# Kernel optimization log

Measured on AMD Instinct MI355X. Metric: run time of the kernel, lower is better.

## Reference

```python
import jax, jax.numpy as jnp
import numpy as np

NUM_NODES = 50000
NUM_EDGES = 600000
NUM_FEAT = 128
HIDDEN = 512
N_OUT = 128
K = 3
N_GRAPHS = 128


def setup_inputs() -> dict:
    key = jax.random.key(0)
    ks = jax.random.split(key, 12)
    feature = jax.random.normal(ks[0], (NUM_NODES, NUM_FEAT), dtype=jnp.float32)
    edge_index = jax.random.randint(ks[1], (2, NUM_EDGES), 0, NUM_NODES, dtype=jnp.int64)
    protein_batch = jnp.sort(jax.random.randint(ks[2], (NUM_NODES,), 0, N_GRAPHS, dtype=jnp.int64))
    s = 0.05
    # ChebConv weights stored [K, in, out] (x @ W), single shared bias per conv
    W1 = jax.random.normal(ks[3], (K, NUM_FEAT, NUM_FEAT), dtype=jnp.float32) * s
    b1 = jax.random.normal(ks[4], (NUM_FEAT,), dtype=jnp.float32) * s
    W2 = jax.random.normal(ks[5], (K, NUM_FEAT, 2 * NUM_FEAT), dtype=jnp.float32) * s
    b2 = jax.random.normal(ks[6], (2 * NUM_FEAT,), dtype=jnp.float32) * s
    fc1_w = jax.random.normal(ks[7], (3 * NUM_FEAT, HIDDEN), dtype=jnp.float32) * s
    fc1_b = jax.random.normal(ks[8], (HIDDEN,), dtype=jnp.float32) * s
    fc2_w = jax.random.normal(ks[9], (HIDDEN, N_OUT), dtype=jnp.float32) * s
    fc2_b = jax.random.normal(ks[10], (N_OUT,), dtype=jnp.float32) * s
    return {"feature": feature, "edge_index": edge_index, "protein_batch": protein_batch,
            "W1": W1, "b1": b1, "W2": W2, "b2": b2,
            "fc1_w": fc1_w, "fc1_b": fc1_b, "fc2_w": fc2_w, "fc2_b": fc2_b}


def _cheb_conv(x, src, dst, edge_w, W, b):
    # PyG ChebConv with sym normalization, lambda_max=2 => scaled Laplacian
    # L_hat has zero diagonal and off-diag weights -1/sqrt(d_i d_j) (edge_w).
    def prop(h):
        return jax.ops.segment_sum(edge_w[:, None] * h[src], dst, num_segments=NUM_NODES)

    Tx0 = x
    out = Tx0 @ W[0]
    Tx1 = prop(x)
    out = out + Tx1 @ W[1]
    for k in range(2, W.shape[0]):
        Tx2 = 2.0 * prop(Tx1) - Tx0
        out = out + Tx2 @ W[k]
        Tx0, Tx1 = Tx1, Tx2
    return out + b


def reference(feature, edge_index, protein_batch, W1, b1, W2, b2, fc1_w, fc1_b, fc2_w, fc2_b):
    src, dst = edge_index[0], edge_index[1]
    deg = jax.ops.segment_sum(jnp.ones_like(src, dtype=feature.dtype), src, num_segments=NUM_NODES)
    dinv = jnp.where(deg > 0, jax.lax.rsqrt(jnp.maximum(deg, 1.0)), 0.0)
    edge_w = -dinv[src] * dinv[dst]  # (2/lambda_max)*L_sym off-diagonal; diag cancels to 0

    gx = jax.nn.relu(_cheb_conv(feature, src, dst, edge_w, W1, b1))
    gx = jax.nn.relu(_cheb_conv(gx, src, dst, edge_w, W2, b2))
    gx = jnp.concatenate([gx, feature], axis=1)  # [N, 3*F]

    # global_mean_pool
    sums = jax.ops.segment_sum(gx, protein_batch, num_segments=N_GRAPHS)
    cnts = jax.ops.segment_sum(jnp.ones((gx.shape[0],), gx.dtype), protein_batch, num_segments=N_GRAPHS)
    pooled = sums / jnp.maximum(cnts, 1.0)[:, None]

    h = jax.nn.relu(pooled @ fc1_w + fc1_b)  # dropout is identity in eval
    return h @ fc2_w + fc2_b
```

## Files before the change

kernel.cpp:

```cpp
#include <hip/hip_runtime.h>
#include <hip/hip_bf16.h>

#define NNODES 50000
#define NEDGES 600000
#define NB 196
#define NBKT 196
#define SB 192
#define SCH (NEDGES / SB)

typedef short vs8 __attribute__((ext_vector_type(8)));
typedef float floatx4 __attribute__((ext_vector_type(4)));

__device__ __forceinline__ float us2f(unsigned short u) {
    unsigned int x = ((unsigned int)u) << 16;
    float f;
    __builtin_memcpy(&f, &x, 4);
    return f;
}
__device__ __forceinline__ unsigned short f2us(float f) {
    unsigned int x;
    __builtin_memcpy(&x, &f, 4);
    unsigned int r = x + 0x7fffu + ((x >> 16) & 1u);
    return (unsigned short)(r >> 16);
}
__device__ __forceinline__ float ldf(const void* p, int i, int ff) {
    if (ff) return us2f(((const unsigned short*)p)[i]);
    return ((const float*)p)[i];
}
__device__ __forceinline__ int2 ldnt_sw(const int2* p) {
    unsigned long long v =
        __builtin_nontemporal_load(reinterpret_cast<const unsigned long long*>(p));
    int2 r;
    r.x = (int)(unsigned int)(v & 0xffffffffULL);
    r.y = (int)(unsigned int)(v >> 32);
    return r;
}
__device__ __forceinline__ void gload_lds16(const unsigned short* g, unsigned short* l) {
    __builtin_amdgcn_global_load_lds(
        (const __attribute__((address_space(1))) unsigned int*)g,
        (__attribute__((address_space(3))) unsigned int*)l, 16, 0, 0);
}
__device__ __forceinline__ void accum8(float w, uint4 u, float& a0, float& a1,
                                       float& a2, float& a3, float& a4, float& a5,
                                       float& a6, float& a7) {
    a0 += w * us2f((unsigned short)(u.x & 0xffffu));
    a1 += w * us2f((unsigned short)(u.x >> 16));
    a2 += w * us2f((unsigned short)(u.y & 0xffffu));
    a3 += w * us2f((unsigned short)(u.y >> 16));
    a4 += w * us2f((unsigned short)(u.z & 0xffffu));
    a5 += w * us2f((unsigned short)(u.z >> 16));
    a6 += w * us2f((unsigned short)(u.w & 0xffffu));
    a7 += w * us2f((unsigned short)(u.w >> 16));
}

__global__ void k_detect(const int* ei, const unsigned int* fw, int* iflag, int* fflag) {
    int lane = threadIdx.x;
    int odd1 = ei[2 * lane + 1];
    int odd2 = ei[128 + 2 * lane + 1];
    unsigned long long nz = __ballot(odd1 != 0 || odd2 != 0);
    unsigned int e = (fw[lane] >> 7) & 0xffu;
    unsigned long long h = __ballot(e > 100u && e < 160u);
    if (lane == 0) {
        *iflag = (nz == 0ULL) ? 1 : 0;
        *fflag = (__popcll(h) > 40) ? 1 : 0;
    }
}

__global__ void k_init(const int* pb, const int* iflag, int* b32, float* psum) {
    int i = blockIdx.x * 256 + threadIdx.x;
    if (i < NNODES) {
        int f = *iflag;
        b32[i] = pb[((size_t)i) << f];
    }
    if (i < 128 * 384) psum[i] = 0.f;
}

__global__ __launch_bounds__(256) void k_deghist(const int* ei, const int* iflag,
                                                 unsigned int* degpart, int* cntpart) {
    __shared__ unsigned int h[25000];
    __shared__ int c[NBKT];
    int t = threadIdx.x, blk = blockIdx.x;
    for (int i = t; i < 25000; i += 256) h[i] = 0u;
    if (t < NBKT) c[t] = 0;
    __syncthreads();
    int f = *iflag;
    int e0 = blk * SCH;
    for (int j = t; j < SCH; j += 256) {
        int e = e0 + j;
        int s = ei[((size_t)e) << f];
        int d = ei[((size_t)(NEDGES + e)) << f];
        atomicAdd(&h[s >> 1], (s & 1) ? 65536u : 1u);
        atomicAdd(&c[d >> 8], 1);
    }
    __syncthreads();
    unsigned int* dp = degpart + (size_t)blk * 25000;
    for (int i = t; i < 25000; i += 256) dp[i] = h[i];
    if (t < NBKT) cntpart[blk * NBKT + t] = c[t];
}

__global__ void k_dred(const unsigned int* degpart, float* dinv) {
    int i = blockIdx.x * 256 + threadIdx.x;
    if (i >= 25000) return;
    unsigned int lo = 0, hi = 0;
    for (int b = 0; b < SB; ++b) {
        unsigned int p = degpart[(size_t)b * 25000 + i];
        lo += p & 0xffffu;
        hi += p >> 16;
    }
    dinv[2 * i] = lo ? rsqrtf((float)lo) : 0.f;
    dinv[2 * i + 1] = hi ? rsqrtf((float)hi) : 0.f;
}

__global__ void k_bscan(const int* cntpart, int* bbase, int* gbase,
                        const int* batch32, int* pcnt, int* rowptr) {
    __shared__ int tot[256];
    int t = threadIdx.x;
    int sum = 0;
    if (t < NBKT) {
        for (int b = 0; b < SB; ++b) sum += cntpart[b * NBKT + t];
    }
    tot[t] = sum;
    __syncthreads();
    for (int off = 1; off < 256; off <<= 1) {
        int x = (t >= off) ? tot[t - off] : 0;
        __syncthreads();
        tot[t] += x;
        __syncthreads();
    }
    int excl = tot[t] - sum;
    if (t < NBKT) {
        gbase[t] = excl;
        int run = excl;
        for (int b = 0; b < SB; ++b) {
            bbase[b * NBKT + t] = run;
            run += cntpart[b * NBKT + t];
        }
    }
    if (t == 0) {
        gbase[NBKT] = NEDGES;
        rowptr[NNODES] = NEDGES;
    }
    if (t < 128) {
        int g = t;
        int lo = 0, hi = NNODES;
        while (lo < hi) { int mid = (lo + hi) >> 1; if (batch32[mid] < g) lo = mid + 1; else hi = mid; }
        int start = lo;
        hi = NNODES;
        while (lo < hi) { int mid = (lo + hi) >> 1; if (batch32[mid] <= g) lo = mid + 1; else hi = mid; }
        pcnt[g] = lo - start;
    }
}

__global__ void k_scat(const int* ei, const int* iflag, const float* dinv,
                       const int* bbase, int2* bkt) {
    __shared__ int cur[NBKT];
    int t = threadIdx.x, blk = blockIdx.x;
    if (t < NBKT) cur[t] = bbase[blk * NBKT + t];
    __syncthreads();
    int f = *iflag;
    int e0 = blk * SCH;
    for (int j = t; j < SCH; j += 256) {
        int e = e0 + j;
        int s = ei[((size_t)e) << f];
        int d = ei[((size_t)(NEDGES + e)) << f];
        float w = -dinv[s] * dinv[d];
        int slot = atomicAdd(&cur[d >> 8], 1);
        int wb;
        __builtin_memcpy(&wb, &w, 4);
        int2 v;
        v.x = s | ((d & 255) << 16);
        v.y = wb;
        bkt[slot] = v;
    }
}

__global__ void k_csr(const int2* bkt, const int* gbase, int* rowptr, int2* csr_sw) {
    __shared__ int hist[256], scan[256], cur[256];
    int t = threadIdx.x, b = blockIdx.x;
    int beg = gbase[b], end = gbase[b + 1];
    int n = end - beg;
    hist[t] = 0;
    __syncthreads();
    for (int i = t; i < n; i += 256) {
        int bin = (bkt[beg + i].x >> 16) & 255;
        atomicAdd(&hist[bin], 1);
    }
    __syncthreads();
    int h = hist[t];
    scan[t] = h;
    __syncthreads();
    for (int off = 1; off < 256; off <<= 1) {
        int x = (t >= off) ? scan[t - off] : 0;
        __syncthreads();
        scan[t] += x;
        __syncthreads();
    }
    int excl = scan[t] - h;
    int node = b * 256 + t;
    if (node < NNODES) rowptr[node] = beg + excl;
    cur[t] = excl;
    __syncthreads();
    for (int i = t; i < n; i += 256) {
        int2 p = bkt[beg + i];
        int bin = (p.x >> 16) & 255;
        int slot = atomicAdd(&cur[bin], 1);
        int2 v;
        v.x = p.x & 0xffff;
        v.y = p.y;
        csr_sw[beg + slot] = v;
    }
}

__global__ void k_featb(const void* src, const int* fflag, unsigned short* dst) {
    int i = blockIdx.x * 256 + threadIdx.x;
    if (i >= NNODES * 128 / 8) return;
    if (*fflag) {
        reinterpret_cast<uint4*>(dst)[i] = reinterpret_cast<const uint4*>(src)[i];
    } else {
        const float4* fs = reinterpret_cast<const float4*>(src);
        float4 a = fs[2 * i], b = fs[2 * i + 1];
        uint4 o;
        o.x = (unsigned int)f2us(a.x) | ((unsigned int)f2us(a.y) << 16);
        o.y = (unsigned int)f2us(a.z) | ((unsigned int)f2us(a.w) << 16);
        o.z = (unsigned int)f2us(b.x) | ((unsigned int)f2us(b.y) << 16);
        o.w = (unsigned int)f2us(b.z) | ((unsigned int)f2us(b.w) << 16);
        reinterpret_cast<uint4*>(dst)[i] = o;
    }
}

__global__ void k_trans2(const void* W1, const void* W2, const int* fflag,
                         unsigned short* W1t, unsigned short* W2t) {
    int idx = blockIdx.x * 256 + threadIdx.x;
    int ff = *fflag;
    if (idx < 49152) {
        int c = idx >> 13;
        int rem = idx & 8191;
        int cr = rem >> 6;
        int rem2 = rem & 63;
        int g = rem2 >> 3, j = rem2 & 7;
        int k = c * 64 + ((g ^ (cr & 7)) << 3) + j;
        int n = cr;
        float v;
        if (k < 128) v = ldf(W1, k * 128 + n, ff) - ldf(W1, (256 + k) * 128 + n, ff);
        else if (k < 256) v = ldf(W1, k * 128 + n, ff);
        else v = 2.f * ldf(W1, k * 128 + n, ff);
        W1t[idx] = f2us(v);
    } else if (idx < 49152 + 98304) {
        int jx = idx - 49152;
        int ct = jx / 49152;
        int rem = jx % 49152;
        int c = rem >> 13;
        int rem1 = rem & 8191;
        int cr = rem1 >> 6;
        int rem2 = rem1 & 63;
        int g = rem2 >> 3, j = rem2 & 7;
        int k = c * 64 + ((g ^ (cr & 7)) << 3) + j;
        int n = ct * 128 + cr;
        float v;
        if (k < 128) v = ldf(W2, k * 256 + n, ff) - ldf(W2, (256 + k) * 256 + n, ff);
        else if (k < 256) v = ldf(W2, k * 256 + n, ff);
        else v = 2.f * ldf(W2, k * 256 + n, ff);
        W2t[jx] = f2us(v);
    }
}

__global__ void k_prepw(const void* b1, const void* b2, const void* f1w, const void* f1b,
                        const void* f2w, const void* f2b, const int* fflag,
                        float* b1f, float* b2f, float* f1wf, float* f1bf,
                        float* f2wf, float* f2bf) {
    int i = blockIdx.x * 256 + threadIdx.x;
    int ff = *fflag;
    if (i < 196608) { f1wf[i] = ldf(f1w, i, ff); return; }
    i -= 196608;
    if (i < 65536) { f2wf[i] = ldf(f2w, i, ff); return; }
    i -= 65536;
    if (i < 512) { f1bf[i] = ldf(f1b, i, ff); return; }
    i -= 512;
    if (i < 256) { b2f[i] = ldf(b2, i, ff); return; }
    i -= 256;
    if (i < 128) { b1f[i] = ldf(b1, i, ff); return; }
    i -= 128;
    if (i < 128) f2bf[i] = ldf(f2b, i, ff);
}

__global__ __launch_bounds__(256, 8) void k_prop(const unsigned short* X,
                                                 const int* rowptr, const int2* csr_sw,
                                                 unsigned short* out) {
    int wvid = (blockIdx.x * blockDim.x + threadIdx.x) >> 6;
    int lane = threadIdx.x & 63;
    int q = lane >> 4;
    int ln = lane & 15;
    int node = wvid * 4 + q;
    if (node >= NNODES) return;
    int fo = ln * 8;
    int beg = rowptr[node], end = rowptr[node + 1];
    float a0 = 0.f, a1 = 0.f, a2 = 0.f, a3 = 0.f;
    float a4 = 0.f, a5 = 0.f, a6 = 0.f, a7 = 0.f;
    int j = beg;
    for (; j + 4 <= end; j += 4) {
        int2 e0 = ldnt_sw(csr_sw + j);
        int2 e1 = ldnt_sw(csr_sw + j + 1);
        int2 e2 = ldnt_sw(csr_sw + j + 2);
        int2 e3 = ldnt_sw(csr_sw + j + 3);
        uint4 u0 = *reinterpret_cast<const uint4*>(X + (size_t)e0.x * 128 + fo);
        uint4 u1 = *reinterpret_cast<const uint4*>(X + (size_t)e1.x * 128 + fo);
        uint4 u2 = *reinterpret_cast<const uint4*>(X + (size_t)e2.x * 128 + fo);
        uint4 u3 = *reinterpret_cast<const uint4*>(X + (size_t)e3.x * 128 + fo);
        float w0, w1, w2, w3;
        __builtin_memcpy(&w0, &e0.y, 4);
        __builtin_memcpy(&w1, &e1.y, 4);
        __builtin_memcpy(&w2, &e2.y, 4);
        __builtin_memcpy(&w3, &e3.y, 4);
        accum8(w0, u0, a0, a1, a2, a3, a4, a5, a6, a7);
        accum8(w1, u1, a0, a1, a2, a3, a4, a5, a6, a7);
        accum8(w2, u2, a0, a1, a2, a3, a4, a5, a6, a7);
        accum8(w3, u3, a0, a1, a2, a3, a4, a5, a6, a7);
    }
    for (; j < end; ++j) {
        int2 e = ldnt_sw(csr_sw + j);
        float w;
        __builtin_memcpy(&w, &e.y, 4);
        uint4 u = *reinterpret_cast<const uint4*>(X + (size_t)e.x * 128 + fo);
        accum8(w, u, a0, a1, a2, a3, a4, a5, a6, a7);
    }
    uint4 ov;
    ov.x = (unsigned int)f2us(a0) | ((unsigned int)f2us(a1) << 16);
    ov.y = (unsigned int)f2us(a2) | ((unsigned int)f2us(a3) << 16);
    ov.z = (unsigned int)f2us(a4) | ((unsigned int)f2us(a5) << 16);
    ov.w = (unsigned int)f2us(a6) | ((unsigned int)f2us(a7) << 16);
    *reinterpret_cast<uint4*>(out + (size_t)node * 128 + fo) = ov;
}

template <int POOL, int CT>
__global__ __launch_bounds__(512, 4) void k_convg(
    const unsigned short* seg0, const unsigned short* seg1, const unsigned short* seg2,
    const unsigned short* Wt, const float* bias, unsigned short* out,
    const int* batch32, float* psum) {
    __shared__ __align__(16) unsigned short a_lds[2][8192];
    __shared__ __align__(16) unsigned short b_lds[2][8192];
    __shared__ float sh_ps[POOL ? 1024 : 1];
    int tid = threadIdx.x;
    int bid = blockIdx.x;
    int grp = 8 * CT;
    int main_blocks = 48 * grp;
    int r, ct;
    if (bid < main_blocks) {
        int g = bid / grp;
        int rem = bid - g * grp;
        ct = rem >> 3;
        r = g * 8 + (rem & 7);
    } else {
        int t = bid - main_blocks;
        r = 384 + (CT == 1 ? t : t % 7);
        ct = (CT == 1) ? 0 : t / 7;
    }
    int r0 = r * 128;
    const unsigned short* segs[3] = {seg0, seg1, seg2};
    int wv = tid >> 6, lane = tid & 63;
    int wm = wv >> 2, wn = wv & 3;
    int m = lane & 15, kq = lane >> 4;
    if (POOL) { sh_ps[tid] = 0.f; sh_ps[tid + 512] = 0.f; }

    auto STAGE = [&](int buf, int c) {
        const unsigned short* S = segs[c >> 1];
        int h = c & 1;
#pragma unroll
        for (int p = 0; p < 2; ++p) {
            int q = wv * 2 + p;
            int rl = q * 8 + (lane >> 3);
            int g = lane & 7;
            int rowg = r0 + rl;
            if (rowg >= NNODES) rowg = NNODES - 1;
            gload_lds16(S + (size_t)rowg * 128 + h * 64 + ((g ^ (rl & 7)) << 3),
                        &a_lds[buf][q * 512]);
        }
#pragma unroll
        for (int p = 0; p < 2; ++p) {
            int q = wv * 2 + p;
            gload_lds16(Wt + (size_t)(ct * 6 + c) * 8192 + q * 512 + (lane << 3),
                        &b_lds[buf][q * 512]);
        }
    };

    floatx4 acc[4][2];
#pragma unroll
    for (int mt = 0; mt < 4; ++mt)
#pragma unroll
        for (int nt = 0; nt < 2; ++nt) {
            acc[mt][nt][0] = 0.f; acc[mt][nt][1] = 0.f;
            acc[mt][nt][2] = 0.f; acc[mt][nt][3] = 0.f;
        }

    STAGE(0, 0);
    __syncthreads();
    int buf = 0;
#pragma unroll
    for (int c = 0; c < 6; ++c) {
        if (c < 5) STAGE(buf ^ 1, c + 1);
        vs8 af[4], bfr[2];
#pragma unroll
        for (int kf = 0; kf < 2; ++kf) {
            int G = kf * 4 + kq;
#pragma unroll
            for (int mt = 0; mt < 4; ++mt) {
                int row = wm * 64 + mt * 16 + m;
                af[mt] = *reinterpret_cast<const vs8*>(
                    &a_lds[buf][row * 64 + ((G ^ (row & 7)) << 3)]);
            }
#pragma unroll
            for (int nt = 0; nt < 2; ++nt) {
                int cl = wn * 32 + nt * 16 + m;
                bfr[nt] = *reinterpret_cast<const vs8*>(
                    &b_lds[buf][cl * 64 + ((G ^ (cl & 7)) << 3)]);
            }
#pragma unroll
            for (int mt = 0; mt < 4; ++mt)
#pragma unroll
                for (int nt = 0; nt < 2; ++nt)
                    acc[mt][nt] = __builtin_amdgcn_mfma_f32_16x16x32_bf16(
                        af[mt], bfr[nt], acc[mt][nt], 0, 0, 0);
        }
        if (c < 5) {
            __syncthreads();
            buf ^= 1;
        }
    }

    if (POOL == 0) {
#pragma unroll
        for (int mt = 0; mt < 4; ++mt) {
            int rbase = r0 + wm * 64 + mt * 16 + kq * 4;
#pragma unroll
            for (int nt = 0; nt < 2; ++nt) {
                int col = wn * 32 + nt * 16 + m;
                float bv = bias[col];
#pragma unroll
                for (int i = 0; i < 4; ++i) {
                    int rw = rbase + i;
                    if (rw < NNODES) {
                        float v = acc[mt][nt][i] + bv;
                        v = v > 0.f ? v : 0.f;
                        out[(size_t)rw * 128 + col] = f2us(v);
                    }
                }
            }
        }
    } else {
        int g0 = batch32[r0];
#pragma unroll
        for (int mt = 0; mt < 4; ++mt) {
            int rbase = r0 + wm * 64 + mt * 16 + kq * 4;
            int gid[4];
#pragma unroll
            for (int i = 0; i < 4; ++i) {
                int rw = rbase + i;
                gid[i] = rw < NNODES ? batch32[rw] : -1;
            }
#pragma unroll
            for (int nt = 0; nt < 2; ++nt) {
                int cl = wn * 32 + nt * 16 + m;
                int col = ct * 128 + cl;
                float bv = bias[col];
                float run = 0.f;
                int curg = -1;
#pragma unroll
                for (int i = 0; i < 4; ++i) {
                    int g = gid[i];
                    if (g < 0) break;
                    float v = acc[mt][nt][i] + bv;
                    v = v > 0.f ? v : 0.f;
                    if (g != curg) {
                        if (curg >= 0) {
                            int gl = curg - g0;
                            if (gl >= 0 && gl < 8) atomicAdd(&sh_ps[gl * 128 + cl], run);
                            else atomicAdd(&psum[curg * 384 + col], run);
                        }
                        curg = g;
                        run = 0.f;
                    }
                    run += v;
                }
                if (curg >= 0) {
                    int gl = curg - g0;
                    if (gl >= 0 && gl < 8) atomicAdd(&sh_ps[gl * 128 + cl], run);
                    else atomicAdd(&psum[curg * 384 + col], run);
                }
            }
        }
        __syncthreads();
        for (int idx = tid; idx < 1024; idx += 512) {
            int gl = idx >> 7, cl = idx & 127;
            float v = sh_ps[idx];
            int gg = g0 + gl;
            if (v != 0.f && gg < 128) atomicAdd(&psum[(size_t)gg * 384 + ct * 128 + cl], v);
        }
    }
}

__global__ void k_poolnodes(const unsigned short* featb, const int* batch32, float* psum) {
    int col = threadIdx.x & 127;
    int half = threadIdx.x >> 7;
    int nbeg = blockIdx.x * 128 + half * 64;
    if (nbeg >= NNODES) return;
    int nend = nbeg + 64;
    if (nend > NNODES) nend = NNODES;
    float run = 0.f;
    int curg = batch32[nbeg];
    for (int n = nbeg; n < nend; ++n) {
        int g = batch32[n];
        if (g != curg) {
            atomicAdd(&psum[curg * 384 + 256 + col], run);
            run = 0.f;
            curg = g;
        }
        run += us2f(featb[(size_t)n * 128 + col]);
    }
    atomicAdd(&psum[curg * 384 + 256 + col], run);
}

__global__ void k_fc1(const float* psum, const int* pcnt, const float* w,
                      const float* b, float* h) {
    int g = blockIdx.x, j = threadIdx.x * 2;
    int c = pcnt[g];
    float inv = 1.f / (float)(c > 0 ? c : 1);
    float a0 = 0.f, a1 = 0.f;
    for (int k = 0; k < 384; ++k) {
        float p = psum[g * 384 + k];
        a0 += p * w[k * 512 + j];
        a1 += p * w[k * 512 + j + 1];
    }
    a0 = a0 * inv + b[j];
    a1 = a1 * inv + b[j + 1];
    h[g * 512 + j] = a0 > 0.f ? a0 : 0.f;
    h[g * 512 + j + 1] = a1 > 0.f ? a1 : 0.f;
}

__global__ void ChebModel_74380243632480_kernel(const float* h, const float* w,
                                                const float* b, const int* fflag,
                                                void* out) {
    int g = blockIdx.x, j = threadIdx.x;
    float acc = 0.f;
    for (int k = 0; k < 512; ++k) acc += h[g * 512 + k] * w[k * 128 + j];
    acc += b[j];
    if (*fflag) ((unsigned short*)out)[g * 128 + j] = f2us(acc);
    else ((float*)out)[g * 128 + j] = acc;
}

extern "C" void kernel_launch(void* const* d_in, const int* in_sizes, int n_in,
                              void* d_out, int out_size, void* d_ws, size_t ws_size,
                              hipStream_t stream) {
    const void* feature = d_in[0];
    const int* edge_index = (const int*)d_in[1];
    const int* batch = (const int*)d_in[2];
    const void* W1 = d_in[3];
    const void* b1 = d_in[4];
    const void* W2 = d_in[5];
    const void* b2 = d_in[6];
    const void* fc1w = d_in[7];
    const void* fc1b = d_in[8];
    const void* fc2w = d_in[9];
    const void* fc2b = d_in[10];

    char* ws = (char*)d_ws;
    size_t off = 0;
    int* iflag = (int*)(ws + off); off += 256;
    int* fflag = (int*)(ws + off); off += 256;
    int* rowptr = (int*)(ws + off); off += ((size_t)(NNODES + 1) * 4 + 255) & ~(size_t)255;
    float* dinv = (float*)(ws + off); off += ((size_t)NNODES * 4 + 255) & ~(size_t)255;
    int* batch32 = (int*)(ws + off); off += ((size_t)NNODES * 4 + 255) & ~(size_t)255;
    int* gbase = (int*)(ws + off); off += 1024;
    int* cntpart = (int*)(ws + off); off += ((size_t)SB * NBKT * 4 + 255) & ~(size_t)255;
    int* bbase = (int*)(ws + off); off += ((size_t)SB * NBKT * 4 + 255) & ~(size_t)255;
    int2* csr_sw = (int2*)(ws + off); off += ((size_t)NEDGES * 8 + 255) & ~(size_t)255;
    unsigned short* featb = (unsigned short*)(ws + off); off += ((size_t)NNODES * 128 * 2 + 255) & ~(size_t)255;
    unsigned short* T1 = (unsigned short*)(ws + off); off += ((size_t)NNODES * 128 * 2 + 255) & ~(size_t)255;
    unsigned short* T2 = (unsigned short*)(ws + off); off += ((size_t)NNODES * 128 * 2 + 255) & ~(size_t)255;
    unsigned short* gx1 = (unsigned short*)(ws + off); off += ((size_t)NNODES * 128 * 2 + 255) & ~(size_t)255;
    unsigned short* W1t = (unsigned short*)(ws + off); off += ((size_t)49152 * 2 + 255) & ~(size_t)255;
    unsigned short* W2t = (unsigned short*)(ws + off); off += ((size_t)98304 * 2 + 255) & ~(size_t)255;
    float* b1f = (float*)(ws + off); off += 1024;
    float* b2f = (float*)(ws + off); off += 1024;
    float* fc1wf = (float*)(ws + off); off += ((size_t)196608 * 4 + 255) & ~(size_t)255;
    float* fc1bf = (float*)(ws + off); off += 2048;
    float* fc2wf = (float*)(ws + off); off += ((size_t)65536 * 4 + 255) & ~(size_t)255;
    float* fc2bf = (float*)(ws + off); off += 1024;
    float* psum = (float*)(ws + off); off += ((size_t)128 * 384 * 4 + 255) & ~(size_t)255;
    int* pcnt = (int*)(ws + off); off += 1024;
    float* hbuf = (float*)(ws + off); off += ((size_t)128 * 512 * 4 + 255) & ~(size_t)255;

    int2* bkt = (int2*)T1;
    unsigned int* degpart = (unsigned int*)T2;

    k_detect<<<1, 64, 0, stream>>>(edge_index, (const unsigned int*)feature, iflag, fflag);
    k_init<<<(NNODES + 255) / 256, 256, 0, stream>>>(batch, iflag, batch32, psum);
    k_deghist<<<SB, 256, 0, stream>>>(edge_index, iflag, degpart, cntpart);
    k_dred<<<(25000 + 255) / 256, 256, 0, stream>>>(degpart, dinv);
    k_bscan<<<1, 256, 0, stream>>>(cntpart, bbase, gbase, batch32, pcnt, rowptr);
    k_scat<<<SB, 256, 0, stream>>>(edge_index, iflag, dinv, bbase, bkt);
    k_csr<<<NBKT, 256, 0, stream>>>(bkt, gbase, rowptr, csr_sw);

    k_featb<<<(NNODES * 128 / 8 + 255) / 256, 256, 0, stream>>>(feature, fflag, featb);
    k_trans2<<<(49152 + 98304 + 255) / 256, 256, 0, stream>>>(W1, W2, fflag, W1t, W2t);
    k_prepw<<<(263168 + 255) / 256, 256, 0, stream>>>(b1, b2, fc1w, fc1b, fc2w, fc2b, fflag,
                                                      b1f, b2f, fc1wf, fc1bf, fc2wf, fc2bf);

    int pb = ((NNODES + 3) / 4 * 64 + 255) / 256;
    k_prop<<<pb, 256, 0, stream>>>(featb, rowptr, csr_sw, T1);
    k_prop<<<pb, 256, 0, stream>>>(T1, rowptr, csr_sw, T2);
    k_convg<0, 1><<<391, 512, 0, stream>>>(featb, T1, T2, W1t, b1f, gx1,
                                           (const int*)0, (float*)0);
    k_prop<<<pb, 256, 0, stream>>>(gx1, rowptr, csr_sw, T1);
    k_prop<<<pb, 256, 0, stream>>>(T1, rowptr, csr_sw, T2);
    k_convg<1, 2><<<782, 512, 0, stream>>>(gx1, T1, T2, W2t, b2f, (unsigned short*)0,
                                           batch32, psum);
    k_poolnodes<<<(NNODES + 127) / 128, 256, 0, stream>>>(featb, batch32, psum);
    k_fc1<<<128, 256, 0, stream>>>(psum, pcnt, fc1wf, fc1bf, hbuf);
    ChebModel_74380243632480_kernel<<<128, 128, 0, stream>>>(hbuf, fc2wf, fc2bf, fflag, d_out);
}
```

Measured before the change: 393.1 us.

## Fuse setup kernels, parallelize bucket prefix scan, unroll SpMM gather by eight

Merges the batch/psum init into the feature bf16 conversion kernel and the three weight-prep kernels into one, cutting kernel launches. Replaces the single-block serial per-bucket scan over 192 partitions with a transposed count layout, a parallel per-bucket prefix kernel and a small global scan, so k_scat computes its base offsets directly. The propagation kernel gains an 8-way unrolled edge loop with more gathers in flight, and its launch-bounds occupancy hint drops from 8 to 6 to leave room for the extra registers. The risks are higher register pressure and lower occupancy in the hot gather kernel.

Result: faster. 367.2 us (-6.6%).

```diff
diff --git a/kernel.cpp b/kernel.cpp
--- a/kernel.cpp
+++ b/kernel.cpp
@@ -66,17 +66,31 @@
     }
 }
 
-__global__ void k_init(const int* pb, const int* iflag, int* b32, float* psum) {
+__global__ void k_featb(const void* src, const int* iflag, const int* fflag,
+                        const int* pb, int* b32, float* psum, unsigned short* dst) {
     int i = blockIdx.x * 256 + threadIdx.x;
     if (i < NNODES) {
         int f = *iflag;
         b32[i] = pb[((size_t)i) << f];
     }
     if (i < 128 * 384) psum[i] = 0.f;
+    if (i >= NNODES * 128 / 8) return;
+    if (*fflag) {
+        reinterpret_cast<uint4*>(dst)[i] = reinterpret_cast<const uint4*>(src)[i];
+    } else {
+        const float4* fs = reinterpret_cast<const float4*>(src);
+        float4 a = fs[2 * i], b = fs[2 * i + 1];
+        uint4 o;
+        o.x = (unsigned int)f2us(a.x) | ((unsigned int)f2us(a.y) << 16);
+        o.y = (unsigned int)f2us(a.z) | ((unsigned int)f2us(a.w) << 16);
+        o.z = (unsigned int)f2us(b.x) | ((unsigned int)f2us(b.y) << 16);
+        o.w = (unsigned int)f2us(b.z) | ((unsigned int)f2us(b.w) << 16);
+        reinterpret_cast<uint4*>(dst)[i] = o;
+    }
 }
 
 __global__ __launch_bounds__(256) void k_deghist(const int* ei, const int* iflag,
-                                                 unsigned int* degpart, int* cntpart) {
+                                                 unsigned int* degpart, int* cntT) {
     __shared__ unsigned int h[25000];
     __shared__ int c[NBKT];
     int t = threadIdx.x, blk = blockIdx.x;
@@ -95,7 +109,7 @@
     __syncthreads();
     unsigned int* dp = degpart + (size_t)blk * 25000;
     for (int i = t; i < 25000; i += 256) dp[i] = h[i];
-    if (t < NBKT) cntpart[blk * NBKT + t] = c[t];
+    if (t < NBKT) cntT[t * SB + blk] = c[t];
 }
 
 __global__ void k_dred(const unsigned int* degpart, float* dinv) {
@@ -111,31 +125,36 @@
     dinv[2 * i + 1] = hi ? rsqrtf((float)hi) : 0.f;
 }
 
-__global__ void k_bscan(const int* cntpart, int* bbase, int* gbase,
-                        const int* batch32, int* pcnt, int* rowptr) {
-    __shared__ int tot[256];
+__global__ void k_bprefix(int* cntT, int* btot) {
+    __shared__ int sh[256];
+    int t = threadIdx.x, b = blockIdx.x;
+    int v = (t < SB) ? cntT[b * SB + t] : 0;
+    sh[t] = v;
+    __syncthreads();
+    for (int off = 1; off < 256; off <<= 1) {
+        int x = (t >= off) ? sh[t - off] : 0;
+        __syncthreads();
+        sh[t] += x;
+        __syncthreads();
+    }
+    if (t < SB) cntT[b * SB + t] = sh[t] - v;
+    if (t == 255) btot[b] = sh[255];
+}
+
+__global__ void k_bscan2(const int* btot, int* gbase, const int* batch32,
+                         int* pcnt, int* rowptr) {
+    __shared__ int sh[256];
     int t = threadIdx.x;
-    int sum = 0;
-    if (t < NBKT) {
-        for (int b = 0; b < SB; ++b) sum += cntpart[b * NBKT + t];
-    }
-    tot[t] = sum;
+    int v = (t < NBKT) ? btot[t] : 0;
+    sh[t] = v;
     __syncthreads();
     for (int off = 1; off < 256; off <<= 1) {
-        int x = (t >= off) ? tot[t - off] : 0;
+        int x = (t >= off) ? sh[t - off] : 0;
         __syncthreads();
-        tot[t] += x;
+        sh[t] += x;
         __syncthreads();
     }
-    int excl = tot[t] - sum;
-    if (t < NBKT) {
-        gbase[t] = excl;
-        int run = excl;
-        for (int b = 0; b < SB; ++b) {
-            bbase[b * NBKT + t] = run;
-            run += cntpart[b * NBKT + t];
-        }
-    }
+    if (t < NBKT) gbase[t] = sh[t] - v;
     if (t == 0) {
         gbase[NBKT] = NEDGES;
         rowptr[NNODES] = NEDGES;
@@ -152,10 +171,10 @@
 }
 
 __global__ void k_scat(const int* ei, const int* iflag, const float* dinv,
-                       const int* bbase, int2* bkt) {
+                       const int* gbase, const int* cntT, int2* bkt) {
     __shared__ int cur[NBKT];
     int t = threadIdx.x, blk = blockIdx.x;
-    if (t < NBKT) cur[t] = bbase[blk * NBKT + t];
+    if (t < NBKT) cur[t] = gbase[t] + cntT[t * SB + blk];
     __syncthreads();
     int f = *iflag;
     int e0 = blk * SCH;
@@ -211,30 +230,16 @@
     }
 }
 
-__global__ void k_featb(const void* src, const int* fflag, unsigned short* dst) {
+__global__ void k_prepall(const void* W1, const void* W2, const void* b1, const void* b2,
+                          const void* f1w, const void* f1b, const void* f2w, const void* f2b,
+                          const int* fflag, unsigned short* W1t, unsigned short* W2t,
+                          float* b1f, float* b2f, float* f1wf, float* f1bf,
+                          float* f2wf, float* f2bf) {
     int i = blockIdx.x * 256 + threadIdx.x;
-    if (i >= NNODES * 128 / 8) return;
-    if (*fflag) {
-        reinterpret_cast<uint4*>(dst)[i] = reinterpret_cast<const uint4*>(src)[i];
-    } else {
-        const float4* fs = reinterpret_cast<const float4*>(src);
-        float4 a = fs[2 * i], b = fs[2 * i + 1];
-        uint4 o;
-        o.x = (unsigned int)f2us(a.x) | ((unsigned int)f2us(a.y) << 16);
-        o.y = (unsigned int)f2us(a.z) | ((unsigned int)f2us(a.w) << 16);
-        o.z = (unsigned int)f2us(b.x) | ((unsigned int)f2us(b.y) << 16);
-        o.w = (unsigned int)f2us(b.z) | ((unsigned int)f2us(b.w) << 16);
-        reinterpret_cast<uint4*>(dst)[i] = o;
-    }
-}
-
-__global__ void k_trans2(const void* W1, const void* W2, const int* fflag,
-                         unsigned short* W1t, unsigned short* W2t) {
-    int idx = blockIdx.x * 256 + threadIdx.x;
     int ff = *fflag;
-    if (idx < 49152) {
-        int c = idx >> 13;
-        int rem = idx & 8191;
+    if (i < 49152) {
+        int c = i >> 13;
+        int rem = i & 8191;
         int cr = rem >> 6;
         int rem2 = rem & 63;
         int g = rem2 >> 3, j = rem2 & 7;
@@ -244,11 +249,13 @@
         if (k < 128) v = ldf(W1, k * 128 + n, ff) - ldf(W1, (256 + k) * 128 + n, ff);
         else if (k < 256) v = ldf(W1, k * 128 + n, ff);
         else v = 2.f * ldf(W1, k * 128 + n, ff);
-        W1t[idx] = f2us(v);
-    } else if (idx < 49152 + 98304) {
-        int jx = idx - 49152;
-        int ct = jx / 49152;
-        int rem = jx % 49152;
+        W1t[i] = f2us(v);
+        return;
+    }
+    i -= 49152;
+    if (i < 98304) {
+        int ct = i / 49152;
+        int rem = i % 49152;
         int c = rem >> 13;
         int rem1 = rem & 8191;
         int cr = rem1 >> 6;
@@ -260,16 +267,10 @@
         if (k < 128) v = ldf(W2, k * 256 + n, ff) - ldf(W2, (256 + k) * 256 + n, ff);
         else if (k < 256) v = ldf(W2, k * 256 + n, ff);
         else v = 2.f * ldf(W2, k * 256 + n, ff);
-        W2t[jx] = f2us(v);
-    }
-}
-
-__global__ void k_prepw(const void* b1, const void* b2, const void* f1w, const void* f1b,
-                        const void* f2w, const void* f2b, const int* fflag,
-                        float* b1f, float* b2f, float* f1wf, float* f1bf,
-                        float* f2wf, float* f2bf) {
-    int i = blockIdx.x * 256 + threadIdx.x;
-    int ff = *fflag;
+        W2t[i] = f2us(v);
+        return;
+    }
+    i -= 98304;
     if (i < 196608) { f1wf[i] = ldf(f1w, i, ff); return; }
     i -= 196608;
     if (i < 65536) { f2wf[i] = ldf(f2w, i, ff); return; }
@@ -283,7 +284,7 @@
     if (i < 128) f2bf[i] = ldf(f2b, i, ff);
 }
 
-__global__ __launch_bounds__(256, 8) void k_prop(const unsigned short* X,
+__global__ __launch_bounds__(256, 6) void k_prop(const unsigned short* X,
                                                  const int* rowptr, const int2* csr_sw,
                                                  unsigned short* out) {
     int wvid = (blockIdx.x * blockDim.x + threadIdx.x) >> 6;
@@ -297,6 +298,41 @@
     float a0 = 0.f, a1 = 0.f, a2 = 0.f, a3 = 0.f;
     float a4 = 0.f, a5 = 0.f, a6 = 0.f, a7 = 0.f;
     int j = beg;
+    for (; j + 8 <= end; j += 8) {
+        int2 e0 = ldnt_sw(csr_sw + j);
+        int2 e1 = ldnt_sw(csr_sw + j + 1);
+        int2 e2 = ldnt_sw(csr_sw + j + 2);
+        int2 e3 = ldnt_sw(csr_sw + j + 3);
+        int2 e4 = ldnt_sw(csr_sw + j + 4);
+        int2 e5 = ldnt_sw(csr_sw + j + 5);
+        int2 e6 = ldnt_sw(csr_sw + j + 6);
+        int2 e7 = ldnt_sw(csr_sw + j + 7);
+        uint4 u0 = *reinterpret_cast<const uint4*>(X + (size_t)e0.x * 128 + fo);
+        uint4 u1 = *reinterpret_cast<const uint4*>(X + (size_t)e1.x * 128 + fo);
+        uint4 u2 = *reinterpret_cast<const uint4*>(X + (size_t)e2.x * 128 + fo);
+        uint4 u3 = *reinterpret_cast<const uint4*>(X + (size_t)e3.x * 128 + fo);
+        uint4 u4 = *reinterpret_cast<const uint4*>(X + (size_t)e4.x * 128 + fo);
+        uint4 u5 = *reinterpret_cast<const uint4*>(X + (size_t)e5.x * 128 + fo);
+        uint4 u6 = *reinterpret_cast<const uint4*>(X + (size_t)e6.x * 128 + fo);
+        uint4 u7 = *reinterpret_cast<const uint4*>(X + (size_t)e7.x * 128 + fo);
+        float w0, w1, w2, w3, w4, w5, w6, w7;
+        __builtin_memcpy(&w0, &e0.y, 4);
+        __builtin_memcpy(&w1, &e1.y, 4);
+        __builtin_memcpy(&w2, &e2.y, 4);
+        __builtin_memcpy(&w3, &e3.y, 4);
+        __builtin_memcpy(&w4, &e4.y, 4);
+        __builtin_memcpy(&w5, &e5.y, 4);
+        __builtin_memcpy(&w6, &e6.y, 4);
+        __builtin_memcpy(&w7, &e7.y, 4);
+        accum8(w0, u0, a0, a1, a2, a3, a4, a5, a6, a7);
+        accum8(w1, u1, a0, a1, a2, a3, a4, a5, a6, a7);
+        accum8(w2, u2, a0, a1, a2, a3, a4, a5, a6, a7);
+        accum8(w3, u3, a0, a1, a2, a3, a4, a5, a6, a7);
+        accum8(w4, u4, a0, a1, a2, a3, a4, a5, a6, a7);
+        accum8(w5, u5, a0, a1, a2, a3, a4, a5, a6, a7);
+        accum8(w6, u6, a0, a1, a2, a3, a4, a5, a6, a7);
+        accum8(w7, u7, a0, a1, a2, a3, a4, a5, a6, a7);
+    }
     for (; j + 4 <= end; j += 4) {
         int2 e0 = ldnt_sw(csr_sw + j);
         int2 e1 = ldnt_sw(csr_sw + j + 1);
@@ -569,8 +605,8 @@
     float* dinv = (float*)(ws + off); off += ((size_t)NNODES * 4 + 255) & ~(size_t)255;
     int* batch32 = (int*)(ws + off); off += ((size_t)NNODES * 4 + 255) & ~(size_t)255;
     int* gbase = (int*)(ws + off); off += 1024;
-    int* cntpart = (int*)(ws + off); off += ((size_t)SB * NBKT * 4 + 255) & ~(size_t)255;
-    int* bbase = (int*)(ws + off); off += ((size_t)SB * NBKT * 4 + 255) & ~(size_t)255;
+    int* cntT = (int*)(ws + off); off += ((size_t)SB * NBKT * 4 + 255) & ~(size_t)255;
+    int* btot = (int*)(ws + off); off += 1024;
     int2* csr_sw = (int2*)(ws + off); off += ((size_t)NEDGES * 8 + 255) & ~(size_t)255;
     unsigned short* featb = (unsigned short*)(ws + off); off += ((size_t)NNODES * 128 * 2 + 255) & ~(size_t)255;
     unsigned short* T1 = (unsigned short*)(ws + off); off += ((size_t)NNODES * 128 * 2 + 255) & ~(size_t)255;
@@ -592,17 +628,17 @@
     unsigned int* degpart = (unsigned int*)T2;
 
     k_detect<<<1, 64, 0, stream>>>(edge_index, (const unsigned int*)feature, iflag, fflag);
-    k_init<<<(NNODES + 255) / 256, 256, 0, stream>>>(batch, iflag, batch32, psum);
-    k_deghist<<<SB, 256, 0, stream>>>(edge_index, iflag, degpart, cntpart);
+    k_featb<<<(NNODES * 128 / 8 + 255) / 256, 256, 0, stream>>>(
+        feature, iflag, fflag, batch, batch32, psum, featb);
+    k_deghist<<<SB, 256, 0, stream>>>(edge_index, iflag, degpart, cntT);
     k_dred<<<(25000 + 255) / 256, 256, 0, stream>>>(degpart, dinv);
-    k_bscan<<<1, 256, 0, stream>>>(cntpart, bbase, gbase, batch32, pcnt, rowptr);
-    k_scat<<<SB, 256, 0, stream>>>(edge_index, iflag, dinv, bbase, bkt);
+    k_bprefix<<<NBKT, 256, 0, stream>>>(cntT, btot);
+    k_bscan2<<<1, 256, 0, stream>>>(btot, gbase, batch32, pcnt, rowptr);
+    k_scat<<<SB, 256, 0, stream>>>(edge_index, iflag, dinv, gbase, cntT, bkt);
     k_csr<<<NBKT, 256, 0, stream>>>(bkt, gbase, rowptr, csr_sw);
-
-    k_featb<<<(NNODES * 128 / 8 + 255) / 256, 256, 0, stream>>>(feature, fflag, featb);
-    k_trans2<<<(49152 + 98304 + 255) / 256, 256, 0, stream>>>(W1, W2, fflag, W1t, W2t);
-    k_prepw<<<(263168 + 255) / 256, 256, 0, stream>>>(b1, b2, fc1w, fc1b, fc2w, fc2b, fflag,
-                                                      b1f, b2f, fc1wf, fc1bf, fc2wf, fc2bf);
+    k_prepall<<<(410624 + 255) / 256, 256, 0, stream>>>(
+        W1, W2, b1, b2, fc1w, fc1b, fc2w, fc2b, fflag,
+        W1t, W2t, b1f, b2f, fc1wf, fc1bf, fc2wf, fc2bf);
 
     int pb = ((NNODES + 3) / 4 * 64 + 255) / 256;
     k_prop<<<pb, 256, 0, stream>>>(featb, rowptr, csr_sw, T1);
```
